# Kernel tuning notes

Measured on AMD Instinct MI355X. Metric: run time of the kernel, lower is better.

Reference implementation:

```python
import jax, jax.numpy as jnp
import numpy as np

T, B, F, H, O = 512, 1024, 16, 32, 8  # seq_len, batch, input_size, hidden, classes


def setup_inputs() -> dict:
    key = jax.random.key(0)
    ks = jax.random.split(key, 11)
    s = 1.0 / np.sqrt(H)  # PyTorch LSTM/Linear uniform init scale
    u = lambda k, shp: jax.random.uniform(k, shp, jnp.float32, -s, s)
    return {
        "x": jax.random.normal(ks[0], (T, B, F), jnp.float32),
        "W_ih_f": u(ks[1], (4 * H, F)),
        "W_hh_f": u(ks[2], (4 * H, H)),
        "b_f": u(ks[3], (4 * H,)),  # combined b_ih + b_hh
        "W_ih_b": u(ks[4], (4 * H, F)),
        "W_hh_b": u(ks[5], (4 * H, H)),
        "b_b": u(ks[6], (4 * H,)),
        "W_fc_h": u(ks[7], (O, 2 * H)),
        "b_fc_h": u(ks[8], (O,)),
        "W_fc_o": jax.random.uniform(ks[9], (O, B * O), jnp.float32, -1 / np.sqrt(B * O), 1 / np.sqrt(B * O)),
        "b_fc_o": u(ks[10], (O,)),
    }


def _lstm_final_hidden(x, W_ih, W_hh, b):
    """Run one LSTM direction over x:(T,B,F); return final hidden h:(B,H)."""
    h_dim = W_hh.shape[1]
    # precompute input contribution for all timesteps: (T, B, 4H)
    gates_x = jnp.einsum('tbf,gf->tbg', x, W_ih) + b

    def step(carry, gx):
        h, c = carry
        g = gx + h @ W_hh.T  # (B, 4H), PyTorch gate order i,f,g,o
        i, f, gg, o = jnp.split(g, 4, axis=-1)
        c = jax.nn.sigmoid(f) * c + jax.nn.sigmoid(i) * jnp.tanh(gg)
        h = jax.nn.sigmoid(o) * jnp.tanh(c)
        return (h, c), None

    bsz = x.shape[1]
    init = (jnp.zeros((bsz, h_dim), x.dtype), jnp.zeros((bsz, h_dim), x.dtype))
    (h, _), _ = jax.lax.scan(step, init, gates_x)
    return h


def reference(x, W_ih_f, W_hh_f, b_f, W_ih_b, W_hh_b, b_b,
              W_fc_h, b_fc_h, W_fc_o, b_fc_o):
    h_fwd = _lstm_final_hidden(x, W_ih_f, W_hh_f, b_f)          # hidden_state[-2]
    h_bwd = _lstm_final_hidden(x[::-1], W_ih_b, W_hh_b, b_b)    # hidden_state[-1]
    hidden = jnp.concatenate([h_fwd, h_bwd], axis=1)            # (B, 2H)
    hidden_fc = hidden @ W_fc_h.T + b_fc_h                      # (B, O)
    flat = hidden_fc.reshape(-1)                                # (B*O,) == flat_dim
    out = W_fc_o @ flat + b_fc_o                                # (O,)
    return jax.nn.softmax(out)
```

## Files before the change

### kernel.cpp

```cpp
#include <hip/hip_runtime.h>

#define TT 512
#define BB 1024
#define FF 16
#define HH 32
#define OO 8
#define CH 16

typedef float v2f __attribute__((ext_vector_type(2)));

__device__ __forceinline__ float rcp_fast(float x) { return __builtin_amdgcn_rcpf(x); }
__device__ __forceinline__ float sigm2(float y) {
    return rcp_fast(1.0f + __builtin_amdgcn_exp2f(-y));
}

#define PIN13(a,b,c,d,e,f,g,h,i,j,k,l,m) \
    asm volatile("" : "+v"(a),"+v"(b),"+v"(c),"+v"(d),"+v"(e),"+v"(f),"+v"(g), \
                      "+v"(h),"+v"(i),"+v"(j),"+v"(k),"+v"(l),"+v"(m))

__global__ __launch_bounds__(64, 2)
void lstm_seq_kernel(const float* __restrict__ x,
                     const float* __restrict__ Wih_f, const float* __restrict__ Whh_f,
                     const float* __restrict__ b_f,
                     const float* __restrict__ Wih_b, const float* __restrict__ Whh_b,
                     const float* __restrict__ b_b,
                     float* __restrict__ hidden)
{
    const int bid  = blockIdx.x;
    const int dir  = bid >> 10;
    const int bb   = bid & (BB - 1);
    const int lane = threadIdx.x;
    const int hi   = lane >> 5;
    const int kk   = lane & 31;

    const float* __restrict__ Wih  = dir ? Wih_b : Wih_f;
    const float* __restrict__ Whh  = dir ? Whh_b : Whh_f;
    const float* __restrict__ bias = dir ? b_b   : b_f;

    const float LOG2E  = 1.4426950408889634f;
    const float L2E2   = 2.0f * LOG2E;

    v2f wi[4][4];
    v2f wh[4][8];
    v2f pb2[4];
#pragma unroll
    for (int g = 0; g < 4; ++g) {
        const float sc = (g == 2) ? L2E2 : LOG2E;
        const int row = kk + g * HH;
        const float4* pi = (const float4*)(Wih + row * FF + hi * 8);
        float4 a = pi[0], b = pi[1];
        wi[g][0] = (v2f){a.x * sc, a.y * sc}; wi[g][1] = (v2f){a.z * sc, a.w * sc};
        wi[g][2] = (v2f){b.x * sc, b.y * sc}; wi[g][3] = (v2f){b.z * sc, b.w * sc};
        const float4* ph = (const float4*)(Whh + row * HH + hi * 16);
        float4 c0 = ph[0], c1 = ph[1], c2 = ph[2], c3 = ph[3];
        wh[g][0] = (v2f){c0.x * sc, c0.y * sc}; wh[g][1] = (v2f){c0.z * sc, c0.w * sc};
        wh[g][2] = (v2f){c1.x * sc, c1.y * sc}; wh[g][3] = (v2f){c1.z * sc, c1.w * sc};
        wh[g][4] = (v2f){c2.x * sc, c2.y * sc}; wh[g][5] = (v2f){c2.z * sc, c2.w * sc};
        wh[g][6] = (v2f){c3.x * sc, c3.y * sc}; wh[g][7] = (v2f){c3.z * sc, c3.w * sc};
        pb2[g] = (v2f){hi ? 0.0f : bias[row] * sc, 0.0f};
    }

    __shared__ __align__(16) float xsb[2 * CH * FF];
    __shared__ __align__(16) float hsb[2 * HH];

    const int sl = lane >> 2;
    const int wl = lane & 3;
    const int t0 = dir ? (TT - 1 - sl) : sl;
    const float* xp = x + (size_t)t0 * (BB * FF) + (size_t)bb * FF + wl * 4;
    const ptrdiff_t dstep = (dir ? -(ptrdiff_t)CH : (ptrdiff_t)CH) * (BB * FF);

    {
        float4 f0 = *(const float4*)xp;
        *(float4*)(xsb + sl * FF + wl * 4) = f0;
    }
    xp += dstep;
    if (hi == 0) hsb[kk] = 0.0f;
    __syncthreads();

    float c = 0.0f, h = 0.0f;

    for (int ci = 0; ci < TT / CH; ++ci) {
        const bool more = (ci + 1 < TT / CH);
        float4 nf;
        if (more) { nf = *(const float4*)xp; xp += dstep; }

        const int xbase = (ci & 1) * (CH * FF) + hi * 8;
#pragma unroll
        for (int tt = 0; tt < CH; ++tt) {
            PIN13(wi[0][0], wi[0][1], wi[0][2], wi[0][3],
                  wi[1][0], wi[1][1], wi[1][2], wi[1][3],
                  wi[2][0], wi[2][1], wi[2][2], wi[2][3], pb2[0]);
            PIN13(wi[3][0], wi[3][1], wi[3][2], wi[3][3],
                  wh[0][0], wh[0][1], wh[0][2], wh[0][3],
                  wh[0][4], wh[0][5], wh[0][6], wh[0][7], pb2[1]);
            PIN13(wh[1][0], wh[1][1], wh[1][2], wh[1][3],
                  wh[1][4], wh[1][5], wh[1][6], wh[1][7],
                  wh[2][0], wh[2][1], wh[2][2], wh[2][3], pb2[2]);
            PIN13(wh[2][4], wh[2][5], wh[2][6], wh[2][7],
                  wh[3][0], wh[3][1], wh[3][2], wh[3][3],
                  wh[3][4], wh[3][5], wh[3][6], wh[3][7], pb2[3]);

            const v2f* xv = (const v2f*)(xsb + xbase + tt * FF);
            const v2f xp0 = xv[0], xp1 = xv[1], xp2 = xv[2], xp3 = xv[3];
            const v2f* hv = (const v2f*)(hsb + (tt & 1) * HH + hi * 16);
            const v2f hp0 = hv[0], hp1 = hv[1], hp2 = hv[2], hp3 = hv[3];
            const v2f hp4 = hv[4], hp5 = hv[5], hp6 = hv[6], hp7 = hv[7];

            v2f a0 = __builtin_elementwise_fma(xp0, wi[0][0], pb2[0]);
            v2f a1 = __builtin_elementwise_fma(xp0, wi[1][0], pb2[1]);
            v2f a2 = __builtin_elementwise_fma(xp0, wi[2][0], pb2[2]);
            v2f a3 = __builtin_elementwise_fma(xp0, wi[3][0], pb2[3]);
            a0 = __builtin_elementwise_fma(xp1, wi[0][1], a0);
            a1 = __builtin_elementwise_fma(xp1, wi[1][1], a1);
            a2 = __builtin_elementwise_fma(xp1, wi[2][1], a2);
            a3 = __builtin_elementwise_fma(xp1, wi[3][1], a3);
            a0 = __builtin_elementwise_fma(xp2, wi[0][2], a0);
            a1 = __builtin_elementwise_fma(xp2, wi[1][2], a1);
            a2 = __builtin_elementwise_fma(xp2, wi[2][2], a2);
            a3 = __builtin_elementwise_fma(xp2, wi[3][2], a3);
            a0 = __builtin_elementwise_fma(xp3, wi[0][3], a0);
            a1 = __builtin_elementwise_fma(xp3, wi[1][3], a1);
            a2 = __builtin_elementwise_fma(xp3, wi[2][3], a2);
            a3 = __builtin_elementwise_fma(xp3, wi[3][3], a3);

            a0 = __builtin_elementwise_fma(hp0, wh[0][0], a0);
            a1 = __builtin_elementwise_fma(hp0, wh[1][0], a1);
            a2 = __builtin_elementwise_fma(hp0, wh[2][0], a2);
            a3 = __builtin_elementwise_fma(hp0, wh[3][0], a3);
            a0 = __builtin_elementwise_fma(hp1, wh[0][1], a0);
            a1 = __builtin_elementwise_fma(hp1, wh[1][1], a1);
            a2 = __builtin_elementwise_fma(hp1, wh[2][1], a2);
            a3 = __builtin_elementwise_fma(hp1, wh[3][1], a3);
            a0 = __builtin_elementwise_fma(hp2, wh[0][2], a0);
            a1 = __builtin_elementwise_fma(hp2, wh[1][2], a1);
            a2 = __builtin_elementwise_fma(hp2, wh[2][2], a2);
            a3 = __builtin_elementwise_fma(hp2, wh[3][2], a3);
            a0 = __builtin_elementwise_fma(hp3, wh[0][3], a0);
            a1 = __builtin_elementwise_fma(hp3, wh[1][3], a1);
            a2 = __builtin_elementwise_fma(hp3, wh[2][3], a2);
            a3 = __builtin_elementwise_fma(hp3, wh[3][3], a3);
            a0 = __builtin_elementwise_fma(hp4, wh[0][4], a0);
            a1 = __builtin_elementwise_fma(hp4, wh[1][4], a1);
            a2 = __builtin_elementwise_fma(hp4, wh[2][4], a2);
            a3 = __builtin_elementwise_fma(hp4, wh[3][4], a3);
            a0 = __builtin_elementwise_fma(hp5, wh[0][5], a0);
            a1 = __builtin_elementwise_fma(hp5, wh[1][5], a1);
            a2 = __builtin_elementwise_fma(hp5, wh[2][5], a2);
            a3 = __builtin_elementwise_fma(hp5, wh[3][5], a3);
            a0 = __builtin_elementwise_fma(hp6, wh[0][6], a0);
            a1 = __builtin_elementwise_fma(hp6, wh[1][6], a1);
            a2 = __builtin_elementwise_fma(hp6, wh[2][6], a2);
            a3 = __builtin_elementwise_fma(hp6, wh[3][6], a3);
            a0 = __builtin_elementwise_fma(hp7, wh[0][7], a0);
            a1 = __builtin_elementwise_fma(hp7, wh[1][7], a1);
            a2 = __builtin_elementwise_fma(hp7, wh[2][7], a2);
            a3 = __builtin_elementwise_fma(hp7, wh[3][7], a3);

            float g0 = a0.x + a0.y;
            float g1 = a1.x + a1.y;
            float g2 = a2.x + a2.y;
            float g3 = a3.x + a3.y;
            g0 += __shfl_xor(g0, 32);
            g1 += __shfl_xor(g1, 32);
            g2 += __shfl_xor(g2, 32);
            g3 += __shfl_xor(g3, 32);

            const float si = sigm2(g0);
            const float sf = sigm2(g1);
            const float tg = fmaf(2.0f, sigm2(g2), -1.0f);
            const float so = sigm2(g3);
            c = fmaf(sf, c, si * tg);
            const float th = fmaf(2.0f, sigm2(L2E2 * c), -1.0f);
            h = so * th;

            if (tt == CH - 1 && more) {
                *(float4*)(xsb + ((ci + 1) & 1) * (CH * FF) + sl * FF + wl * 4) = nf;
            }
            if (hi == 0) hsb[((tt & 1) ^ 1) * HH + kk] = h;
            __syncthreads();
        }
    }

    if (hi == 0) hidden[(size_t)bb * 64 + dir * HH + kk] = h;
}

__global__ __launch_bounds__(256)
void fc_partial_kernel(const float* __restrict__ hidden,
                       const float* __restrict__ Wfh, const float* __restrict__ bfh,
                       const float* __restrict__ Wfo,
                       float* __restrict__ partials)
{
    __shared__ float wsh[OO * 64];
    const int tid = threadIdx.x;
    for (int i = tid; i < OO * 64; i += 256) wsh[i] = Wfh[i];
    __syncthreads();

    const int r   = tid >> 3;
    const int o   = tid & 7;
    const int row = blockIdx.x * 32 + r;

    const float* hrow = hidden + (size_t)row * 64;
    float acc = bfh[o];
#pragma unroll
    for (int j = 0; j < 64; ++j) acc += hrow[j] * wsh[o * 64 + j];

    const int fidx = blockIdx.x * 256 + tid;

    float pv[OO];
#pragma unroll
    for (int o2 = 0; o2 < OO; ++o2) pv[o2] = Wfo[(size_t)o2 * (BB * OO) + fidx] * acc;

    __shared__ float red[4][OO];
#pragma unroll
    for (int o2 = 0; o2 < OO; ++o2) {
        float v = pv[o2];
        for (int off = 32; off > 0; off >>= 1) v += __shfl_down(v, off);
        if ((tid & 63) == 0) red[tid >> 6][o2] = v;
    }
    __syncthreads();
    if (tid < OO) {
        partials[blockIdx.x * OO + tid] =
            red[0][tid] + red[1][tid] + red[2][tid] + red[3][tid];
    }
}

__global__ void finalize_kernel(const float* __restrict__ partials,
                                const float* __restrict__ bfo,
                                float* __restrict__ out)
{
    __shared__ float s[OO];
    const int tid = threadIdx.x;
    if (tid < OO) {
        float acc = bfo[tid];
        for (int b = 0; b < 32; ++b) acc += partials[b * OO + tid];
        s[tid] = acc;
    }
    __syncthreads();
    if (tid == 0) {
        float m = s[0];
        for (int i = 1; i < OO; ++i) m = fmaxf(m, s[i]);
        float e[OO], sum = 0.0f;
        for (int i = 0; i < OO; ++i) { e[i] = expf(s[i] - m); sum += e[i]; }
        for (int i = 0; i < OO; ++i) out[i] = e[i] / sum;
    }
}

extern "C" void kernel_launch(void* const* d_in, const int* in_sizes, int n_in,
                              void* d_out, int out_size, void* d_ws, size_t ws_size,
                              hipStream_t stream) {
    const float* x     = (const float*)d_in[0];
    const float* Wih_f = (const float*)d_in[1];
    const float* Whh_f = (const float*)d_in[2];
    const float* b_f   = (const float*)d_in[3];
    const float* Wih_b = (const float*)d_in[4];
    const float* Whh_b = (const float*)d_in[5];
    const float* b_b   = (const float*)d_in[6];
    const float* Wfh   = (const float*)d_in[7];
    const float* bfh   = (const float*)d_in[8];
    const float* Wfo   = (const float*)d_in[9];
    const float* bfo   = (const float*)d_in[10];

    float* hidden   = (float*)d_ws;
    float* partials = hidden + (size_t)BB * 64;

    lstm_seq_kernel<<<2 * BB, 64, 0, stream>>>(x, Wih_f, Whh_f, b_f,
                                               Wih_b, Whh_b, b_b, hidden);
    fc_partial_kernel<<<32, 256, 0, stream>>>(hidden, Wfh, bfh, Wfo, partials);
    finalize_kernel<<<1, 64, 0, stream>>>(partials, bfo, (float*)d_out);
}
```

Before: 216.8 us.

## Use fp16 packed dot2 for LSTM gate matmuls with fp32 accumulation

Weights, inputs and the recurrent hidden state are stored as fp16 pairs, and the gate dot products use v_dot2 instructions with fp32 accumulation, replacing the packed fp32 FMAs. This halves the register footprint for weights and the shared-memory traffic for x and h, and uses two independent accumulator chains to shorten the dependency. The hidden state is quantized to fp16 every step over 512 recurrent steps, so rounding error can build up and may break the accuracy tolerance.

```diff
diff --git a/kernel.cpp b/kernel.cpp
--- a/kernel.cpp
+++ b/kernel.cpp
@@ -7,16 +7,21 @@
 #define OO 8
 #define CH 16
 
-typedef float v2f __attribute__((ext_vector_type(2)));
+typedef _Float16 f16;
+typedef f16 v2h __attribute__((ext_vector_type(2)));
+typedef f16 v4h __attribute__((ext_vector_type(4)));
 
 __device__ __forceinline__ float rcp_fast(float x) { return __builtin_amdgcn_rcpf(x); }
 __device__ __forceinline__ float sigm2(float y) {
     return rcp_fast(1.0f + __builtin_amdgcn_exp2f(-y));
 }
-
-#define PIN13(a,b,c,d,e,f,g,h,i,j,k,l,m) \
-    asm volatile("" : "+v"(a),"+v"(b),"+v"(c),"+v"(d),"+v"(e),"+v"(f),"+v"(g), \
-                      "+v"(h),"+v"(i),"+v"(j),"+v"(k),"+v"(l),"+v"(m))
+__device__ __forceinline__ float fdot2(v2h a, v2h b, float c) {
+    return __builtin_amdgcn_fdot2(a, b, c, false);
+}
+
+#define PIN12(a,b,c,d,e,f,g,h,i,j,k,l) \
+    asm volatile("" : "+v"(a),"+v"(b),"+v"(c),"+v"(d),"+v"(e),"+v"(f), \
+                      "+v"(g),"+v"(h),"+v"(i),"+v"(j),"+v"(k),"+v"(l))
 
 __global__ __launch_bounds__(64, 2)
 void lstm_seq_kernel(const float* __restrict__ x,
@@ -37,31 +42,37 @@
     const float* __restrict__ Whh  = dir ? Whh_b : Whh_f;
     const float* __restrict__ bias = dir ? b_b   : b_f;
 
-    const float LOG2E  = 1.4426950408889634f;
-    const float L2E2   = 2.0f * LOG2E;
-
-    v2f wi[4][4];
-    v2f wh[4][8];
-    v2f pb2[4];
+    const float LOG2E = 1.4426950408889634f;
+    const float L2E2  = 2.0f * LOG2E;
+
+    v2h wi[4][4];
+    v2h wh[4][8];
+    float pb[4];
 #pragma unroll
     for (int g = 0; g < 4; ++g) {
         const float sc = (g == 2) ? L2E2 : LOG2E;
         const int row = kk + g * HH;
         const float4* pi = (const float4*)(Wih + row * FF + hi * 8);
-        float4 a = pi[0], b = pi[1];
-        wi[g][0] = (v2f){a.x * sc, a.y * sc}; wi[g][1] = (v2f){a.z * sc, a.w * sc};
-        wi[g][2] = (v2f){b.x * sc, b.y * sc}; wi[g][3] = (v2f){b.z * sc, b.w * sc};
+        float4 a = pi[0], b2 = pi[1];
+        wi[g][0] = (v2h){(f16)(a.x * sc), (f16)(a.y * sc)};
+        wi[g][1] = (v2h){(f16)(a.z * sc), (f16)(a.w * sc)};
+        wi[g][2] = (v2h){(f16)(b2.x * sc), (f16)(b2.y * sc)};
+        wi[g][3] = (v2h){(f16)(b2.z * sc), (f16)(b2.w * sc)};
         const float4* ph = (const float4*)(Whh + row * HH + hi * 16);
         float4 c0 = ph[0], c1 = ph[1], c2 = ph[2], c3 = ph[3];
-        wh[g][0] = (v2f){c0.x * sc, c0.y * sc}; wh[g][1] = (v2f){c0.z * sc, c0.w * sc};
-        wh[g][2] = (v2f){c1.x * sc, c1.y * sc}; wh[g][3] = (v2f){c1.z * sc, c1.w * sc};
-        wh[g][4] = (v2f){c2.x * sc, c2.y * sc}; wh[g][5] = (v2f){c2.z * sc, c2.w * sc};
-        wh[g][6] = (v2f){c3.x * sc, c3.y * sc}; wh[g][7] = (v2f){c3.z * sc, c3.w * sc};
-        pb2[g] = (v2f){hi ? 0.0f : bias[row] * sc, 0.0f};
-    }
-
-    __shared__ __align__(16) float xsb[2 * CH * FF];
-    __shared__ __align__(16) float hsb[2 * HH];
+        wh[g][0] = (v2h){(f16)(c0.x * sc), (f16)(c0.y * sc)};
+        wh[g][1] = (v2h){(f16)(c0.z * sc), (f16)(c0.w * sc)};
+        wh[g][2] = (v2h){(f16)(c1.x * sc), (f16)(c1.y * sc)};
+        wh[g][3] = (v2h){(f16)(c1.z * sc), (f16)(c1.w * sc)};
+        wh[g][4] = (v2h){(f16)(c2.x * sc), (f16)(c2.y * sc)};
+        wh[g][5] = (v2h){(f16)(c2.z * sc), (f16)(c2.w * sc)};
+        wh[g][6] = (v2h){(f16)(c3.x * sc), (f16)(c3.y * sc)};
+        wh[g][7] = (v2h){(f16)(c3.z * sc), (f16)(c3.w * sc)};
+        pb[g] = hi ? 0.0f : bias[row] * sc;
+    }
+
+    __shared__ __align__(8) f16 xsb[2 * CH * FF];
+    __shared__ __align__(8) f16 hsb[2 * HH];
 
     const int sl = lane >> 2;
     const int wl = lane & 3;
@@ -71,10 +82,11 @@
 
     {
         float4 f0 = *(const float4*)xp;
-        *(float4*)(xsb + sl * FF + wl * 4) = f0;
+        *(v4h*)(xsb + sl * FF + wl * 4) =
+            (v4h){(f16)f0.x, (f16)f0.y, (f16)f0.z, (f16)f0.w};
     }
     xp += dstep;
-    if (hi == 0) hsb[kk] = 0.0f;
+    hsb[lane] = (f16)0.0f;
     __syncthreads();
 
     float c = 0.0f, h = 0.0f;
@@ -87,79 +99,78 @@
         const int xbase = (ci & 1) * (CH * FF) + hi * 8;
 #pragma unroll
         for (int tt = 0; tt < CH; ++tt) {
-            PIN13(wi[0][0], wi[0][1], wi[0][2], wi[0][3],
+            PIN12(wi[0][0], wi[0][1], wi[0][2], wi[0][3],
                   wi[1][0], wi[1][1], wi[1][2], wi[1][3],
-                  wi[2][0], wi[2][1], wi[2][2], wi[2][3], pb2[0]);
-            PIN13(wi[3][0], wi[3][1], wi[3][2], wi[3][3],
+                  wi[2][0], wi[2][1], wi[2][2], wi[2][3]);
+            PIN12(wi[3][0], wi[3][1], wi[3][2], wi[3][3],
                   wh[0][0], wh[0][1], wh[0][2], wh[0][3],
-                  wh[0][4], wh[0][5], wh[0][6], wh[0][7], pb2[1]);
-            PIN13(wh[1][0], wh[1][1], wh[1][2], wh[1][3],
+                  wh[0][4], wh[0][5], wh[0][6], wh[0][7]);
+            PIN12(wh[1][0], wh[1][1], wh[1][2], wh[1][3],
                   wh[1][4], wh[1][5], wh[1][6], wh[1][7],
-                  wh[2][0], wh[2][1], wh[2][2], wh[2][3], pb2[2]);
-            PIN13(wh[2][4], wh[2][5], wh[2][6], wh[2][7],
+                  wh[2][0], wh[2][1], wh[2][2], wh[2][3]);
+            PIN12(wh[2][4], wh[2][5], wh[2][6], wh[2][7],
                   wh[3][0], wh[3][1], wh[3][2], wh[3][3],
-                  wh[3][4], wh[3][5], wh[3][6], wh[3][7], pb2[3]);
-
-            const v2f* xv = (const v2f*)(xsb + xbase + tt * FF);
-            const v2f xp0 = xv[0], xp1 = xv[1], xp2 = xv[2], xp3 = xv[3];
-            const v2f* hv = (const v2f*)(hsb + (tt & 1) * HH + hi * 16);
-            const v2f hp0 = hv[0], hp1 = hv[1], hp2 = hv[2], hp3 = hv[3];
-            const v2f hp4 = hv[4], hp5 = hv[5], hp6 = hv[6], hp7 = hv[7];
-
-            v2f a0 = __builtin_elementwise_fma(xp0, wi[0][0], pb2[0]);
-            v2f a1 = __builtin_elementwise_fma(xp0, wi[1][0], pb2[1]);
-            v2f a2 = __builtin_elementwise_fma(xp0, wi[2][0], pb2[2]);
-            v2f a3 = __builtin_elementwise_fma(xp0, wi[3][0], pb2[3]);
-            a0 = __builtin_elementwise_fma(xp1, wi[0][1], a0);
-            a1 = __builtin_elementwise_fma(xp1, wi[1][1], a1);
-            a2 = __builtin_elementwise_fma(xp1, wi[2][1], a2);
-            a3 = __builtin_elementwise_fma(xp1, wi[3][1], a3);
-            a0 = __builtin_elementwise_fma(xp2, wi[0][2], a0);
-            a1 = __builtin_elementwise_fma(xp2, wi[1][2], a1);
-            a2 = __builtin_elementwise_fma(xp2, wi[2][2], a2);
-            a3 = __builtin_elementwise_fma(xp2, wi[3][2], a3);
-            a0 = __builtin_elementwise_fma(xp3, wi[0][3], a0);
-            a1 = __builtin_elementwise_fma(xp3, wi[1][3], a1);
-            a2 = __builtin_elementwise_fma(xp3, wi[2][3], a2);
-            a3 = __builtin_elementwise_fma(xp3, wi[3][3], a3);
-
-            a0 = __builtin_elementwise_fma(hp0, wh[0][0], a0);
-            a1 = __builtin_elementwise_fma(hp0, wh[1][0], a1);
-            a2 = __builtin_elementwise_fma(hp0, wh[2][0], a2);
-            a3 = __builtin_elementwise_fma(hp0, wh[3][0], a3);
-            a0 = __builtin_elementwise_fma(hp1, wh[0][1], a0);
-            a1 = __builtin_elementwise_fma(hp1, wh[1][1], a1);
-            a2 = __builtin_elementwise_fma(hp1, wh[2][1], a2);
-            a3 = __builtin_elementwise_fma(hp1, wh[3][1], a3);
-            a0 = __builtin_elementwise_fma(hp2, wh[0][2], a0);
-            a1 = __builtin_elementwise_fma(hp2, wh[1][2], a1);
-            a2 = __builtin_elementwise_fma(hp2, wh[2][2], a2);
-            a3 = __builtin_elementwise_fma(hp2, wh[3][2], a3);
-            a0 = __builtin_elementwise_fma(hp3, wh[0][3], a0);
-            a1 = __builtin_elementwise_fma(hp3, wh[1][3], a1);
-            a2 = __builtin_elementwise_fma(hp3, wh[2][3], a2);
-            a3 = __builtin_elementwise_fma(hp3, wh[3][3], a3);
-            a0 = __builtin_elementwise_fma(hp4, wh[0][4], a0);
-            a1 = __builtin_elementwise_fma(hp4, wh[1][4], a1);
-            a2 = __builtin_elementwise_fma(hp4, wh[2][4], a2);
-            a3 = __builtin_elementwise_fma(hp4, wh[3][4], a3);
-            a0 = __builtin_elementwise_fma(hp5, wh[0][5], a0);
-            a1 = __builtin_elementwise_fma(hp5, wh[1][5], a1);
-            a2 = __builtin_elementwise_fma(hp5, wh[2][5], a2);
-            a3 = __builtin_elementwise_fma(hp5, wh[3][5], a3);
-            a0 = __builtin_elementwise_fma(hp6, wh[0][6], a0);
-            a1 = __builtin_elementwise_fma(hp6, wh[1][6], a1);
-            a2 = __builtin_elementwise_fma(hp6, wh[2][6], a2);
-            a3 = __builtin_elementwise_fma(hp6, wh[3][6], a3);
-            a0 = __builtin_elementwise_fma(hp7, wh[0][7], a0);
-            a1 = __builtin_elementwise_fma(hp7, wh[1][7], a1);
-            a2 = __builtin_elementwise_fma(hp7, wh[2][7], a2);
-            a3 = __builtin_elementwise_fma(hp7, wh[3][7], a3);
-
-            float g0 = a0.x + a0.y;
-            float g1 = a1.x + a1.y;
-            float g2 = a2.x + a2.y;
-            float g3 = a3.x + a3.y;
+                  wh[3][4], wh[3][5], wh[3][6], wh[3][7]);
+
+            const v2h* xv = (const v2h*)(xsb + xbase + tt * FF);
+            const v2h x0 = xv[0], x1 = xv[1], x2 = xv[2], x3 = xv[3];
+            const v2h* hv = (const v2h*)(hsb + (tt & 1) * HH + hi * 16);
+            const v2h h0 = hv[0], h1 = hv[1], h2 = hv[2], h3 = hv[3];
+            const v2h h4 = hv[4], h5 = hv[5], h6 = hv[6], h7 = hv[7];
+
+            float A0 = fdot2(x0, wi[0][0], pb[0]);
+            float A1 = fdot2(x0, wi[1][0], pb[1]);
+            float A2 = fdot2(x0, wi[2][0], pb[2]);
+            float A3 = fdot2(x0, wi[3][0], pb[3]);
+            float B0 = fdot2(x2, wi[0][2], 0.0f);
+            float B1 = fdot2(x2, wi[1][2], 0.0f);
+            float B2 = fdot2(x2, wi[2][2], 0.0f);
+            float B3 = fdot2(x2, wi[3][2], 0.0f);
+            A0 = fdot2(x1, wi[0][1], A0);
+            A1 = fdot2(x1, wi[1][1], A1);
+            A2 = fdot2(x1, wi[2][1], A2);
+            A3 = fdot2(x1, wi[3][1], A3);
+            B0 = fdot2(x3, wi[0][3], B0);
+            B1 = fdot2(x3, wi[1][3], B1);
+            B2 = fdot2(x3, wi[2][3], B2);
+            B3 = fdot2(x3, wi[3][3], B3);
+            A0 = fdot2(h0, wh[0][0], A0);
+            A1 = fdot2(h0, wh[1][0], A1);
+            A2 = fdot2(h0, wh[2][0], A2);
+            A3 = fdot2(h0, wh[3][0], A3);
+            B0 = fdot2(h4, wh[0][4], B0);
+            B1 = fdot2(h4, wh[1][4], B1);
+            B2 = fdot2(h4, wh[2][4], B2);
+            B3 = fdot2(h4, wh[3][4], B3);
+            A0 = fdot2(h1, wh[0][1], A0);
+            A1 = fdot2(h1, wh[1][1], A1);
+            A2 = fdot2(h1, wh[2][1], A2);
+            A3 = fdot2(h1, wh[3][1], A3);
+            B0 = fdot2(h5, wh[0][5], B0);
+            B1 = fdot2(h5, wh[1][5], B1);
+            B2 = fdot2(h5, wh[2][5], B2);
+            B3 = fdot2(h5, wh[3][5], B3);
+            A0 = fdot2(h2, wh[0][2], A0);
+            A1 = fdot2(h2, wh[1][2], A1);
+            A2 = fdot2(h2, wh[2][2], A2);
+            A3 = fdot2(h2, wh[3][2], A3);
+            B0 = fdot2(h6, wh[0][6], B0);
+            B1 = fdot2(h6, wh[1][6], B1);
+            B2 = fdot2(h6, wh[2][6], B2);
+            B3 = fdot2(h6, wh[3][6], B3);
+            A0 = fdot2(h3, wh[0][3], A0);
+            A1 = fdot2(h3, wh[1][3], A1);
+            A2 = fdot2(h3, wh[2][3], A2);
+            A3 = fdot2(h3, wh[3][3], A3);
+            B0 = fdot2(h7, wh[0][7], B0);
+            B1 = fdot2(h7, wh[1][7], B1);
+            B2 = fdot2(h7, wh[2][7], B2);
+            B3 = fdot2(h7, wh[3][7], B3);
+
+            float g0 = A0 + B0;
+            float g1 = A1 + B1;
+            float g2 = A2 + B2;
+            float g3 = A3 + B3;
             g0 += __shfl_xor(g0, 32);
             g1 += __shfl_xor(g1, 32);
             g2 += __shfl_xor(g2, 32);
@@ -174,9 +185,10 @@
             h = so * th;
 
             if (tt == CH - 1 && more) {
-                *(float4*)(xsb + ((ci + 1) & 1) * (CH * FF) + sl * FF + wl * 4) = nf;
+                *(v4h*)(xsb + ((ci + 1) & 1) * (CH * FF) + sl * FF + wl * 4) =
+                    (v4h){(f16)nf.x, (f16)nf.y, (f16)nf.z, (f16)nf.w};
             }
-            if (hi == 0) hsb[((tt & 1) ^ 1) * HH + kk] = h;
+            hsb[((tt & 1) ^ 1) * HH + kk] = (f16)h;
             __syncthreads();
         }
     }
```

Result: slower. 235.4 us (+8.6%).
